# Optimization experiments

Measured on AMD Instinct MI355X. Metric: run time of the kernel, lower is better.

The kernel has to match this reference:

```python
import jax, jax.numpy as jnp
import numpy as np

# tinygemm asymmetric int4 convention
QUANT_MIN, QUANT_MAX = 0, 15
MID_POINT = (QUANT_MAX + QUANT_MIN + 1) / 2.0  # 8.0
OUT_F, IN_F, GROUP = 8192, 8192, 128
M_TOKENS = 64


def setup_inputs() -> dict:
    key = jax.random.key(0)
    kx, kw = jax.random.split(key)
    x = jax.random.normal(kx, (M_TOKENS, IN_F), dtype=jnp.float32)
    # Materialize quantized params exactly as quantize_weight_tinygemm does.
    w = jax.random.normal(kw, (OUT_F, IN_F), dtype=jnp.float32) * 0.02
    ng = IN_F // GROUP
    wg = w.reshape(OUT_F, ng, GROUP)
    min_val = wg.min(axis=2)
    max_val = wg.max(axis=2)
    scale = jnp.maximum((max_val - min_val) / float(QUANT_MAX - QUANT_MIN), 1.1920929e-7)
    zero_point = min_val + scale * MID_POINT
    min_val_recon = zero_point - scale * MID_POINT
    q = jnp.clip(jnp.round((wg - min_val_recon[..., None]) / scale[..., None]),
                 QUANT_MIN, QUANT_MAX).astype(jnp.int32)
    int_data = q.reshape(OUT_F, IN_F)  # values in [0, 15]
    # tinygemm layout: (n_groups, out_features, 2) with [..., 0]=scale, [..., 1]=zero_point
    scale_and_zero = jnp.stack([scale, zero_point], axis=-1).transpose(1, 0, 2)
    return {"x": x, "int_data": int_data, "scale_and_zero": scale_and_zero}


def reference(x, int_data, scale_and_zero):
    # Dequant: w = (q - MID_POINT) * scale + zero_point, per group of GROUP along in_features.
    ng = IN_F // GROUP
    q = int_data.reshape(OUT_F, ng, GROUP).astype(x.dtype)
    scale = scale_and_zero[..., 0].T[:, :, None]       # (OUT_F, ng, 1)
    zero_point = scale_and_zero[..., 1].T[:, :, None]  # (OUT_F, ng, 1)
    w = ((q - MID_POINT) * scale + zero_point).reshape(OUT_F, IN_F)
    return x @ w.T  # (M, OUT_F)
```

## Files before the change

kernel.cpp:

```cpp
#include <hip/hip_runtime.h>


#define OUT_F 8192
#define IN_F  8192
#define M_TOK 64
#define GROUP 128
#define BN    128
#define KSPLIT 16
#define KR    (IN_F / KSPLIT)

typedef short  short8 __attribute__((ext_vector_type(8)));
typedef float  f32x4  __attribute__((ext_vector_type(4)));

__device__ __forceinline__ unsigned short f2bf(float f) {
    unsigned u = __float_as_uint(f);
    return (unsigned short)((u + 0x7FFFu + ((u >> 16) & 1u)) >> 16);
}

__global__ __launch_bounds__(256, 4)
void woq_linear_kernel(const float* __restrict__ x,
                       const int*   __restrict__ qw,
                       const float* __restrict__ sz,
                       float*       __restrict__ out) {
    __shared__ short lds_x[16 * 64 * 8];

    const int t    = threadIdx.x;
    const int lane = t & 63;
    const int wv   = t >> 6;
    const int n0   = blockIdx.x * BN;
    const int k0   = blockIdx.y * KR;

    const int nlo  = lane & 15;
    const int quad = lane >> 4;
    const int kq8  = quad << 3;

    const int n1 = n0 + wv * 32 + nlo;
    const int n2 = n1 + 16;

    f32x4 acc[4][2];
#pragma unroll
    for (int mi = 0; mi < 4; ++mi)
#pragma unroll
        for (int ni = 0; ni < 2; ++ni)
            acc[mi][ni] = (f32x4){0.f, 0.f, 0.f, 0.f};

    for (int g = 0; g < KR / GROUP; ++g) {
        const int kg = k0 + g * GROUP;
        const int gg = kg >> 7;

        const float2 p1 = *(const float2*)(sz + ((size_t)gg * OUT_F + n1) * 2);
        const float2 p2 = *(const float2*)(sz + ((size_t)gg * OUT_F + n2) * 2);
        const float s1 = p1.x, c1 = fmaf(-8.f, p1.x, p1.y);
        const float s2 = p2.x, c2 = fmaf(-8.f, p2.x, p2.y);

        __syncthreads();
#pragma unroll
        for (int i = 0; i < 4; ++i) {
            int slot  = t + 256 * i;
            int chunk = slot >> 6;
            int l     = slot & 63;
            int m     = ((chunk & 3) << 4) + (l & 15);
            int kk    = ((chunk >> 2) << 5) + ((l >> 4) << 3);
            const float4* p = (const float4*)(x + (size_t)m * IN_F + kg + kk);
            float4 v0 = p[0];
            float4 v1 = p[1];
            short8 bv;
            bv[0] = (short)f2bf(v0.x); bv[1] = (short)f2bf(v0.y);
            bv[2] = (short)f2bf(v0.z); bv[3] = (short)f2bf(v0.w);
            bv[4] = (short)f2bf(v1.x); bv[5] = (short)f2bf(v1.y);
            bv[6] = (short)f2bf(v1.z); bv[7] = (short)f2bf(v1.w);
            *(short8*)&lds_x[slot * 8] = bv;
        }
        __syncthreads();

#pragma unroll
        for (int ks = 0; ks < 4; ++ks) {
            const int k = kg + ks * 32;

            const int* q1p = qw + (size_t)n1 * IN_F + k + kq8;
            const int* q2p = qw + (size_t)n2 * IN_F + k + kq8;
            const int4 qa = *(const int4*)(q1p);
            const int4 qb = *(const int4*)(q1p + 4);
            const int4 qc = *(const int4*)(q2p);
            const int4 qd = *(const int4*)(q2p + 4);

            short8 a[4];
#pragma unroll
            for (int mi = 0; mi < 4; ++mi)
                a[mi] = *(const short8*)&lds_x[((ks * 4 + mi) * 64 + lane) * 8];

            short8 b1, b2;
            b1[0] = (short)f2bf(fmaf((float)qa.x, s1, c1));
            b1[1] = (short)f2bf(fmaf((float)qa.y, s1, c1));
            b1[2] = (short)f2bf(fmaf((float)qa.z, s1, c1));
            b1[3] = (short)f2bf(fmaf((float)qa.w, s1, c1));
            b1[4] = (short)f2bf(fmaf((float)qb.x, s1, c1));
            b1[5] = (short)f2bf(fmaf((float)qb.y, s1, c1));
            b1[6] = (short)f2bf(fmaf((float)qb.z, s1, c1));
            b1[7] = (short)f2bf(fmaf((float)qb.w, s1, c1));
            b2[0] = (short)f2bf(fmaf((float)qc.x, s2, c2));
            b2[1] = (short)f2bf(fmaf((float)qc.y, s2, c2));
            b2[2] = (short)f2bf(fmaf((float)qc.z, s2, c2));
            b2[3] = (short)f2bf(fmaf((float)qc.w, s2, c2));
            b2[4] = (short)f2bf(fmaf((float)qd.x, s2, c2));
            b2[5] = (short)f2bf(fmaf((float)qd.y, s2, c2));
            b2[6] = (short)f2bf(fmaf((float)qd.z, s2, c2));
            b2[7] = (short)f2bf(fmaf((float)qd.w, s2, c2));

#pragma unroll
            for (int mi = 0; mi < 4; ++mi) {
                acc[mi][0] = __builtin_amdgcn_mfma_f32_16x16x32_bf16(a[mi], b1, acc[mi][0], 0, 0, 0);
                acc[mi][1] = __builtin_amdgcn_mfma_f32_16x16x32_bf16(a[mi], b2, acc[mi][1], 0, 0, 0);
            }
        }
    }

#pragma unroll
    for (int mi = 0; mi < 4; ++mi) {
#pragma unroll
        for (int ni = 0; ni < 2; ++ni) {
            const int n = n0 + wv * 32 + ni * 16 + nlo;
#pragma unroll
            for (int r = 0; r < 4; ++r) {
                const int m = mi * 16 + quad * 4 + r;
                atomicAdd(out + (size_t)m * OUT_F + n, acc[mi][ni][r]);
            }
        }
    }
}

extern "C" void kernel_launch(void* const* d_in, const int* in_sizes, int n_in,
                              void* d_out, int out_size, void* d_ws, size_t ws_size,
                              hipStream_t stream) {
    const float* x  = (const float*)d_in[0];
    const int*   qw = (const int*)d_in[1];
    const float* sz = (const float*)d_in[2];
    float* out = (float*)d_out;

    hipMemsetAsync(d_out, 0, (size_t)out_size * sizeof(float), stream);

    dim3 grid(OUT_F / BN, KSPLIT);
    woq_linear_kernel<<<grid, 256, 0, stream>>>(x, qw, sz, out);
}
```

Measured before the change: 402.1 us.

## Replace atomic split-K accumulation with workspace partials and a reduce kernel

```diff
diff --git a/kernel.cpp b/kernel.cpp
--- a/kernel.cpp
+++ b/kernel.cpp
@@ -9,20 +9,23 @@
 #define KSPLIT 16
 #define KR    (IN_F / KSPLIT)
 
-typedef short  short8 __attribute__((ext_vector_type(8)));
-typedef float  f32x4  __attribute__((ext_vector_type(4)));
+typedef short short8 __attribute__((ext_vector_type(8)));
+typedef float f32x4  __attribute__((ext_vector_type(4)));
+typedef int   int4v  __attribute__((ext_vector_type(4)));
 
-__device__ __forceinline__ unsigned short f2bf(float f) {
-    unsigned u = __float_as_uint(f);
-    return (unsigned short)((u + 0x7FFFu + ((u >> 16) & 1u)) >> 16);
+__device__ __forceinline__ int pack_bf2(float lo, float hi) {
+    unsigned ul = __float_as_uint(lo) + 0x8000u;
+    unsigned uh = __float_as_uint(hi) + 0x8000u;
+    return (int)((ul >> 16) | (uh & 0xFFFF0000u));
 }
 
+template <bool ATOMIC>
 __global__ __launch_bounds__(256, 4)
-void woq_linear_kernel(const float* __restrict__ x,
-                       const int*   __restrict__ qw,
-                       const float* __restrict__ sz,
-                       float*       __restrict__ out) {
-    __shared__ short lds_x[16 * 64 * 8];
+void woq_gemm(const float* __restrict__ x,
+              const int*   __restrict__ qw,
+              const float* __restrict__ sz,
+              float*       __restrict__ outp) {
+    __shared__ int lds_x[16 * 64 * 4];
 
     const int t    = threadIdx.x;
     const int lane = t & 63;
@@ -64,12 +67,12 @@
             const float4* p = (const float4*)(x + (size_t)m * IN_F + kg + kk);
             float4 v0 = p[0];
             float4 v1 = p[1];
-            short8 bv;
-            bv[0] = (short)f2bf(v0.x); bv[1] = (short)f2bf(v0.y);
-            bv[2] = (short)f2bf(v0.z); bv[3] = (short)f2bf(v0.w);
-            bv[4] = (short)f2bf(v1.x); bv[5] = (short)f2bf(v1.y);
-            bv[6] = (short)f2bf(v1.z); bv[7] = (short)f2bf(v1.w);
-            *(short8*)&lds_x[slot * 8] = bv;
+            int4v bv;
+            bv.x = pack_bf2(v0.x, v0.y);
+            bv.y = pack_bf2(v0.z, v0.w);
+            bv.z = pack_bf2(v1.x, v1.y);
+            bv.w = pack_bf2(v1.z, v1.w);
+            *(int4v*)&lds_x[slot * 4] = bv;
         }
         __syncthreads();
 
@@ -87,34 +90,30 @@
             short8 a[4];
 #pragma unroll
             for (int mi = 0; mi < 4; ++mi)
-                a[mi] = *(const short8*)&lds_x[((ks * 4 + mi) * 64 + lane) * 8];
+                a[mi] = *(const short8*)&lds_x[((ks * 4 + mi) * 64 + lane) * 4];
 
-            short8 b1, b2;
-            b1[0] = (short)f2bf(fmaf((float)qa.x, s1, c1));
-            b1[1] = (short)f2bf(fmaf((float)qa.y, s1, c1));
-            b1[2] = (short)f2bf(fmaf((float)qa.z, s1, c1));
-            b1[3] = (short)f2bf(fmaf((float)qa.w, s1, c1));
-            b1[4] = (short)f2bf(fmaf((float)qb.x, s1, c1));
-            b1[5] = (short)f2bf(fmaf((float)qb.y, s1, c1));
-            b1[6] = (short)f2bf(fmaf((float)qb.z, s1, c1));
-            b1[7] = (short)f2bf(fmaf((float)qb.w, s1, c1));
-            b2[0] = (short)f2bf(fmaf((float)qc.x, s2, c2));
-            b2[1] = (short)f2bf(fmaf((float)qc.y, s2, c2));
-            b2[2] = (short)f2bf(fmaf((float)qc.z, s2, c2));
-            b2[3] = (short)f2bf(fmaf((float)qc.w, s2, c2));
-            b2[4] = (short)f2bf(fmaf((float)qd.x, s2, c2));
-            b2[5] = (short)f2bf(fmaf((float)qd.y, s2, c2));
-            b2[6] = (short)f2bf(fmaf((float)qd.z, s2, c2));
-            b2[7] = (short)f2bf(fmaf((float)qd.w, s2, c2));
+            int4v b1i, b2i;
+            b1i.x = pack_bf2(fmaf((float)qa.x, s1, c1), fmaf((float)qa.y, s1, c1));
+            b1i.y = pack_bf2(fmaf((float)qa.z, s1, c1), fmaf((float)qa.w, s1, c1));
+            b1i.z = pack_bf2(fmaf((float)qb.x, s1, c1), fmaf((float)qb.y, s1, c1));
+            b1i.w = pack_bf2(fmaf((float)qb.z, s1, c1), fmaf((float)qb.w, s1, c1));
+            short8 b1 = __builtin_bit_cast(short8, b1i);
+#pragma unroll
+            for (int mi = 0; mi < 4; ++mi)
+                acc[mi][0] = __builtin_amdgcn_mfma_f32_16x16x32_bf16(a[mi], b1, acc[mi][0], 0, 0, 0);
 
+            b2i.x = pack_bf2(fmaf((float)qc.x, s2, c2), fmaf((float)qc.y, s2, c2));
+            b2i.y = pack_bf2(fmaf((float)qc.z, s2, c2), fmaf((float)qc.w, s2, c2));
+            b2i.z = pack_bf2(fmaf((float)qd.x, s2, c2), fmaf((float)qd.y, s2, c2));
+            b2i.w = pack_bf2(fmaf((float)qd.z, s2, c2), fmaf((float)qd.w, s2, c2));
+            short8 b2 = __builtin_bit_cast(short8, b2i);
 #pragma unroll
-            for (int mi = 0; mi < 4; ++mi) {
-                acc[mi][0] = __builtin_amdgcn_mfma_f32_16x16x32_bf16(a[mi], b1, acc[mi][0], 0, 0, 0);
+            for (int mi = 0; mi < 4; ++mi)
                 acc[mi][1] = __builtin_amdgcn_mfma_f32_16x16x32_bf16(a[mi], b2, acc[mi][1], 0, 0, 0);
-            }
         }
     }
 
+    float* dst = ATOMIC ? outp : outp + (size_t)blockIdx.y * (M_TOK * OUT_F);
 #pragma unroll
     for (int mi = 0; mi < 4; ++mi) {
 #pragma unroll
@@ -123,10 +122,26 @@
 #pragma unroll
             for (int r = 0; r < 4; ++r) {
                 const int m = mi * 16 + quad * 4 + r;
-                atomicAdd(out + (size_t)m * OUT_F + n, acc[mi][ni][r]);
+                if (ATOMIC)
+                    atomicAdd(dst + (size_t)m * OUT_F + n, acc[mi][ni][r]);
+                else
+                    dst[(size_t)m * OUT_F + n] = acc[mi][ni][r];
             }
         }
     }
+}
+
+__global__ __launch_bounds__(256)
+void woq_reduce(const float* __restrict__ part, float* __restrict__ out) {
+    const int i = (blockIdx.x * 256 + threadIdx.x) * 4;
+    const size_t stride = (size_t)M_TOK * OUT_F;
+    float4 s = *(const float4*)(part + i);
+#pragma unroll
+    for (int k = 1; k < KSPLIT; ++k) {
+        float4 v = *(const float4*)(part + (size_t)k * stride + i);
+        s.x += v.x; s.y += v.y; s.z += v.z; s.w += v.w;
+    }
+    *(float4*)(out + i) = s;
 }
 
 extern "C" void kernel_launch(void* const* d_in, const int* in_sizes, int n_in,
@@ -137,8 +152,15 @@
     const float* sz = (const float*)d_in[2];
     float* out = (float*)d_out;
 
-    hipMemsetAsync(d_out, 0, (size_t)out_size * sizeof(float), stream);
+    dim3 grid(OUT_F / BN, KSPLIT);
+    const size_t need = (size_t)KSPLIT * M_TOK * OUT_F * sizeof(float);
 
-    dim3 grid(OUT_F / BN, KSPLIT);
-    woq_linear_kernel<<<grid, 256, 0, stream>>>(x, qw, sz, out);
+    if (ws_size >= need) {
+        float* part = (float*)d_ws;
+        woq_gemm<false><<<grid, 256, 0, stream>>>(x, qw, sz, part);
+        woq_reduce<<<(M_TOK * OUT_F) / (256 * 4), 256, 0, stream>>>(part, out);
+    } else {
+        hipMemsetAsync(d_out, 0, (size_t)out_size * sizeof(float), stream);
+        woq_gemm<true><<<grid, 256, 0, stream>>>(x, qw, sz, out);
+    }
 }
```

Measured after the change: 390.3 us, median of 2. -2.9%, faster.
